# Kernel tuning notes

Hardware: AMD Instinct MI355X
Metric: run time of the kernel (lower is better)

The kernel has to match this reference:

```python
import jax, jax.numpy as jnp
import numpy as np

N_NODES = 4096
N_EDGES = 128
D_X = 128
PE_DIM = 64
NUM_WALKS = 10
WALK_LEN = 5
EMBED_ROWS = 10000
EDGE_P = 0.02
NEG_INF = -1e30


def setup_inputs() -> dict:
    key = jax.random.key(0)
    kx, kh, ke = jax.random.split(key, 3)
    x = jax.random.normal(kx, (N_NODES, D_X), dtype=jnp.float32)
    # binary hypergraph incidence matrix (float, as used by torch H @ H.T)
    incidence = (jax.random.uniform(kh, (N_NODES, N_EDGES)) < EDGE_P).astype(jnp.float32)
    embed_weight = jax.random.normal(ke, (EMBED_ROWS, PE_DIM), dtype=jnp.float32) * 0.02
    return {"x": x, "incidence": incidence, "embed_weight": embed_weight}


def _sample_walks(neighbors, num_walks, walk_length, key):
    """Vectorized random walks: [W, L] node ids and [W, L] validity mask.

    Matches the torch loop: uniform multinomial over (H@H.T>0) neighbors with
    the self-loop zeroed, terminating early when a node has no neighbors.
    """
    N = neighbors.shape[0]
    nb = jax.lax.stop_gradient(neighbors) * (1.0 - jnp.eye(N, dtype=neighbors.dtype))
    logits = jnp.where(nb > 0, 0.0, NEG_INF)  # uniform over neighbors
    row_has = nb.sum(axis=1) > 0              # probs.sum() == 0 -> break
    starts = jnp.repeat(jnp.arange(N), num_walks)  # [W]
    W = starts.shape[0]

    def step(carry, k):
        cur, alive = carry
        alive = alive & row_has[cur]
        nxt = jax.random.categorical(k, logits[cur])  # [W]
        nxt = jnp.where(alive, nxt, cur)
        return (nxt, alive), (nxt, alive)

    keys = jax.random.split(key, walk_length - 1)
    _, (steps, valid) = jax.lax.scan(step, (starts, jnp.ones((W,), bool)), keys)
    walk_nodes = jnp.concatenate([starts[None, :], steps], axis=0).T     # [W, L]
    valid = jnp.concatenate([jnp.ones((1, W), bool), valid], axis=0).T   # [W, L]
    return walk_nodes, valid


def reference(x, incidence, embed_weight):
    N = x.shape[0]
    # node_neighbors = (H @ H.T > 0).float()
    neighbors = ((incidence @ incidence.T) > 0).astype(x.dtype)  # [N, N]
    walk_nodes, valid = _sample_walks(neighbors, NUM_WALKS, WALK_LEN, jax.random.key(42))

    # mean embedding of each walk over its valid (actual) length
    lens = valid.sum(axis=1).astype(x.dtype)                 # [W], >= 1
    emb = embed_weight[walk_nodes]                           # [W, L, D]
    m = (emb * valid[..., None]).sum(axis=1) / lens[:, None]  # [W, D]

    # every (walk, position) occurrence contributes m_walk to pe[node]
    idx = jnp.where(valid, walk_nodes, 0).reshape(-1)                      # [W*L]
    contrib = jnp.where(valid[..., None], m[:, None, :], 0.0)
    contrib = contrib.reshape(-1, m.shape[-1])                             # [W*L, D]
    w = valid.astype(x.dtype).reshape(-1)
    pe_sum = jax.ops.segment_sum(contrib, idx, num_segments=N)             # [N, D]
    cnt = jax.ops.segment_sum(w, idx, num_segments=N)                      # [N]
    pe = jnp.where(cnt[:, None] > 0, pe_sum / jnp.maximum(cnt, 1.0)[:, None], 0.0)
    return jnp.concatenate([x, pe], axis=-1)
```

## Files before the change

### kernel.cpp

```cpp
#include <hip/hip_runtime.h>
#include <hip/hip_fp16.h>
#include <stdint.h>

#define N_NODES   4096
#define N_EDGES   128
#define D_X       128
#define PE_DIM    64
#define NUM_WALKS 10
#define WALK_LEN  5
#define N_WALKS_TOT (N_NODES * NUM_WALKS)
#define OUT_COLS  (D_X + PE_DIM)
#define ROW_CAP   512u
#define VCAP      512u

#define OFF_MASKS   0u
#define OFF_DEG     (OFF_MASKS + N_NODES * 16u)
#define OFF_ADJ     (OFF_DEG + N_NODES * 4u)
#define OFF_WM      (OFF_ADJ + N_NODES * ROW_CAP * 2u)
#define OFF_VCNT    (OFF_WM + N_WALKS_TOT * PE_DIM * 2u)
#define OFF_VLIST   (OFF_VCNT + N_NODES * 4u)

__device__ __forceinline__ void tf2x32(uint32_t kk0, uint32_t kk1,
                                       uint32_t x0, uint32_t x1,
                                       uint32_t& o0, uint32_t& o1) {
  const uint32_t kk2 = kk0 ^ kk1 ^ 0x1BD11BDAu;
  x0 += kk0; x1 += kk1;
  auto rnd = [&](int r) {
    x0 += x1;
    x1 = (x1 << r) | (x1 >> (32 - r));
    x1 ^= x0;
  };
  rnd(13); rnd(15); rnd(26); rnd(6);   x0 += kk1; x1 += kk2 + 1u;
  rnd(17); rnd(29); rnd(16); rnd(24);  x0 += kk2; x1 += kk0 + 2u;
  rnd(13); rnd(15); rnd(26); rnd(6);   x0 += kk0; x1 += kk1 + 3u;
  rnd(17); rnd(29); rnd(16); rnd(24);  x0 += kk1; x1 += kk2 + 4u;
  rnd(13); rnd(15); rnd(26); rnd(6);   x0 += kk2; x1 += kk0 + 5u;
  o0 = x0; o1 = x1;
}

__global__ void k_masks(const float* __restrict__ inc,
                        ulonglong2* __restrict__ masks,
                        unsigned int* __restrict__ vcnt) {
  const int wid = threadIdx.x >> 6, lane = threadIdx.x & 63;
  const int i = blockIdx.x * 4 + wid;
  const float a = inc[i * N_EDGES + lane];
  const float b = inc[i * N_EDGES + 64 + lane];
  const unsigned long long m0 = __ballot(a != 0.f);
  const unsigned long long m1 = __ballot(b != 0.f);
  if (lane == 0) {
    masks[i] = make_ulonglong2(m0, m1);
    vcnt[i] = 0u;
  }
}

__global__ void __launch_bounds__(512)
k_adj(const ulonglong2* __restrict__ masks,
      unsigned short* __restrict__ adj, unsigned int* __restrict__ deg) {
  __shared__ ulonglong2 sm[N_NODES];
  for (int k = threadIdx.x; k < N_NODES; k += 512) sm[k] = masks[k];
  __syncthreads();
  const int wid = threadIdx.x >> 6, lane = threadIdx.x & 63;
  const int i = blockIdx.x * 8 + wid;
  const ulonglong2 mi = sm[i];
  unsigned short* row = adj + (unsigned int)i * ROW_CAP;
  unsigned int base = 0;
  for (int g = 0; g < N_NODES / 64; ++g) {
    const int j = g * 64 + lane;
    const ulonglong2 mj = sm[j];
    const bool pred = (((mi.x & mj.x) | (mi.y & mj.y)) != 0ull) && (j != i);
    const unsigned long long bal = __ballot(pred);
    if (pred) {
      const unsigned int off =
          (unsigned int)__popcll(bal & ((1ull << lane) - 1ull));
      const unsigned int pos = base + off;
      if (pos < ROW_CAP) row[pos] = (unsigned short)j;
    }
    base += (unsigned int)__popcll(bal);
  }
  if (lane == 0) deg[i] = (base < ROW_CAP) ? base : ROW_CAP;
}

__global__ void __launch_bounds__(256)
k_walk(const unsigned int* __restrict__ deg,
       const unsigned short* __restrict__ adj,
       const float* __restrict__ embed,
       __half* __restrict__ walk_m,
       unsigned int* __restrict__ vcnt, unsigned short* __restrict__ vlist) {
  const int wid = threadIdx.x >> 6, lane = threadIdx.x & 63;
  const int w = blockIdx.x * 4 + wid;

  uint32_t a0, a1;
  tf2x32(0u, 42u, (uint32_t)w, (uint32_t)(lane & 1), a0, a1);
  const uint32_t rnd0 = __shfl(a0, 0);
  const uint32_t rnd1 = __shfl(a1, 0);
  const uint32_t rnd2 = __shfl(a0, 1);
  const uint32_t rnd3 = __shfl(a1, 1);

  const uint32_t n0 = (uint32_t)w / NUM_WALKS;
  uint32_t n1, n2, n3, n4, nvalid;
  const unsigned int d0 = deg[n0];
  if (d0 == 0) {
    n1 = n2 = n3 = n4 = n0;
    nvalid = 1u;
  } else {
    uint32_t cur = n0;
    unsigned int d;
    cur = adj[(cur << 9) + (uint32_t)(((uint64_t)rnd0 * d0) >> 32)]; n1 = cur;
    d = deg[cur];
    cur = adj[(cur << 9) + (uint32_t)(((uint64_t)rnd1 * d) >> 32)]; n2 = cur;
    d = deg[cur];
    cur = adj[(cur << 9) + (uint32_t)(((uint64_t)rnd2 * d) >> 32)]; n3 = cur;
    d = deg[cur];
    cur = adj[(cur << 9) + (uint32_t)(((uint64_t)rnd3 * d) >> 32)]; n4 = cur;
    nvalid = 5u;
  }

  float s = embed[n0 * PE_DIM + lane];
  if (nvalid == 5u) {
    s += embed[n1 * PE_DIM + lane];
    s += embed[n2 * PE_DIM + lane];
    s += embed[n3 * PE_DIM + lane];
    s += embed[n4 * PE_DIM + lane];
  }
  const float m = s / (float)nvalid;

  walk_m[(unsigned int)w * PE_DIM + lane] = __float2half(m);

  if ((unsigned int)lane < nvalid) {
    uint32_t node = n0;
    if (lane == 1) node = n1;
    if (lane == 2) node = n2;
    if (lane == 3) node = n3;
    if (lane == 4) node = n4;
    const unsigned int slot = atomicAdd(&vcnt[node], 1u);
    if (slot < VCAP) vlist[node * VCAP + slot] = (unsigned short)w;
  }
}

__global__ void __launch_bounds__(256)
k_gather(const __half* __restrict__ walk_m,
         const unsigned int* __restrict__ vcnt,
         const unsigned short* __restrict__ vlist,
         const float* __restrict__ x,
         float* __restrict__ out) {
  __shared__ float red[4][PE_DIM];
  const int wid = threadIdx.x >> 6, lane = threadIdx.x & 63;
  const int v = blockIdx.x;

  if (wid == 1) {
    const float2 xv = ((const float2*)(x + (unsigned int)v * D_X))[lane];
    ((float2*)(out + (unsigned int)v * OUT_COLS))[lane] = xv;
  }

  unsigned int c = vcnt[v];
  if (c > VCAP) c = VCAP;
  const unsigned short* vl = vlist + (unsigned int)v * VCAP;

  float s = 0.f;
  for (unsigned int base = (unsigned int)wid * 8u; base < c; base += 32u) {
#pragma unroll
    for (int q = 0; q < 8; ++q) {
      const unsigned int idx = base + (unsigned int)q;
      const bool ok = idx < c;
      const unsigned int ww = ok ? (unsigned int)vl[idx] : (unsigned int)vl[0];
      const float val = __half2float(walk_m[ww * PE_DIM + lane]);
      s += ok ? val : 0.f;
    }
  }
  red[wid][lane] = s;
  __syncthreads();
  if (wid == 0) {
    const float t = red[0][lane] + red[1][lane] + red[2][lane] + red[3][lane];
    out[(unsigned int)v * OUT_COLS + D_X + lane] = c ? t / (float)c : 0.f;
  }
}

extern "C" void kernel_launch(void* const* d_in, const int* in_sizes, int n_in,
                              void* d_out, int out_size, void* d_ws, size_t ws_size,
                              hipStream_t stream) {
  const float* x   = (const float*)d_in[0];
  const float* inc = (const float*)d_in[1];
  const float* emb = (const float*)d_in[2];
  float* out = (float*)d_out;

  char* ws = (char*)d_ws;
  ulonglong2*     masks = (ulonglong2*)(ws + OFF_MASKS);
  unsigned int*   deg   = (unsigned int*)(ws + OFF_DEG);
  unsigned short* adj   = (unsigned short*)(ws + OFF_ADJ);
  __half*         wm    = (__half*)(ws + OFF_WM);
  unsigned int*   vcnt  = (unsigned int*)(ws + OFF_VCNT);
  unsigned short* vlist = (unsigned short*)(ws + OFF_VLIST);

  k_masks <<<N_NODES / 4, 256, 0, stream>>>(inc, masks, vcnt);
  k_adj   <<<N_NODES / 8, 512, 0, stream>>>(masks, adj, deg);
  k_walk  <<<N_WALKS_TOT / 4, 256, 0, stream>>>(deg, adj, emb, wm, vcnt, vlist);
  k_gather<<<N_NODES, 256, 0, stream>>>(wm, vcnt, vlist, x, out);
}
```

Measured before the change: 62.29 us.

## Run one walk per thread and recompute walk means in gather from node records

The walk kernel now maps one walk to a thread instead of one walk to a 64-lane wavefront. It stores a compact 16-byte record of the walk's node ids and valid length, no longer computing and writing a half-precision 64-dim mean per walk. The gather kernel reads these records and re-sums the embedding rows for every walk that visits the node, so the per-walk mean is recomputed up to five times. This removes the fp16 rounding and the large intermediate buffer, but gather now makes about five times as many embedding loads per visit, and the walk kernel's lanes diverge on dependent adjacency lookups.

```diff
diff --git a/kernel.cpp b/kernel.cpp
--- a/kernel.cpp
+++ b/kernel.cpp
@@ -1,5 +1,4 @@
 #include <hip/hip_runtime.h>
-#include <hip/hip_fp16.h>
 #include <stdint.h>
 
 #define N_NODES   4096
@@ -16,9 +15,9 @@
 #define OFF_MASKS   0u
 #define OFF_DEG     (OFF_MASKS + N_NODES * 16u)
 #define OFF_ADJ     (OFF_DEG + N_NODES * 4u)
-#define OFF_WM      (OFF_ADJ + N_NODES * ROW_CAP * 2u)
-#define OFF_VCNT    (OFF_WM + N_WALKS_TOT * PE_DIM * 2u)
+#define OFF_VCNT    (OFF_ADJ + N_NODES * ROW_CAP * 2u)
 #define OFF_VLIST   (OFF_VCNT + N_NODES * 4u)
+#define OFF_WNODES  (OFF_VLIST + N_NODES * VCAP * 2u)
 
 __device__ __forceinline__ void tf2x32(uint32_t kk0, uint32_t kk1,
                                        uint32_t x0, uint32_t x1,
@@ -80,23 +79,18 @@
   if (lane == 0) deg[i] = (base < ROW_CAP) ? base : ROW_CAP;
 }
 
-__global__ void __launch_bounds__(256)
+__global__ void __launch_bounds__(64)
 k_walk(const unsigned int* __restrict__ deg,
        const unsigned short* __restrict__ adj,
-       const float* __restrict__ embed,
-       __half* __restrict__ walk_m,
+       uint4* __restrict__ wnodes,
        unsigned int* __restrict__ vcnt, unsigned short* __restrict__ vlist) {
-  const int wid = threadIdx.x >> 6, lane = threadIdx.x & 63;
-  const int w = blockIdx.x * 4 + wid;
-
-  uint32_t a0, a1;
-  tf2x32(0u, 42u, (uint32_t)w, (uint32_t)(lane & 1), a0, a1);
-  const uint32_t rnd0 = __shfl(a0, 0);
-  const uint32_t rnd1 = __shfl(a1, 0);
-  const uint32_t rnd2 = __shfl(a0, 1);
-  const uint32_t rnd3 = __shfl(a1, 1);
-
-  const uint32_t n0 = (uint32_t)w / NUM_WALKS;
+  const uint32_t w = blockIdx.x * 64u + threadIdx.x;
+
+  uint32_t r0, r1, r2, r3;
+  tf2x32(0u, 42u, w, 0u, r0, r1);
+  tf2x32(0u, 42u, w, 1u, r2, r3);
+
+  const uint32_t n0 = w / NUM_WALKS;
   uint32_t n1, n2, n3, n4, nvalid;
   const unsigned int d0 = deg[n0];
   if (d0 == 0) {
@@ -105,51 +99,51 @@
   } else {
     uint32_t cur = n0;
     unsigned int d;
-    cur = adj[(cur << 9) + (uint32_t)(((uint64_t)rnd0 * d0) >> 32)]; n1 = cur;
+    cur = adj[(cur << 9) + (uint32_t)(((uint64_t)r0 * d0) >> 32)]; n1 = cur;
     d = deg[cur];
-    cur = adj[(cur << 9) + (uint32_t)(((uint64_t)rnd1 * d) >> 32)]; n2 = cur;
+    cur = adj[(cur << 9) + (uint32_t)(((uint64_t)r1 * d) >> 32)]; n2 = cur;
     d = deg[cur];
-    cur = adj[(cur << 9) + (uint32_t)(((uint64_t)rnd2 * d) >> 32)]; n3 = cur;
+    cur = adj[(cur << 9) + (uint32_t)(((uint64_t)r2 * d) >> 32)]; n3 = cur;
     d = deg[cur];
-    cur = adj[(cur << 9) + (uint32_t)(((uint64_t)rnd3 * d) >> 32)]; n4 = cur;
+    cur = adj[(cur << 9) + (uint32_t)(((uint64_t)r3 * d) >> 32)]; n4 = cur;
     nvalid = 5u;
   }
 
-  float s = embed[n0 * PE_DIM + lane];
+  uint4 rec;
+  rec.x = n0 | (n1 << 16);
+  rec.y = n2 | (n3 << 16);
+  rec.z = n4 | (nvalid << 16);
+  rec.w = 0u;
+  wnodes[w] = rec;
+
+  unsigned int s0 = atomicAdd(&vcnt[n0], 1u);
+  if (s0 < VCAP) vlist[n0 * VCAP + s0] = (unsigned short)w;
   if (nvalid == 5u) {
-    s += embed[n1 * PE_DIM + lane];
-    s += embed[n2 * PE_DIM + lane];
-    s += embed[n3 * PE_DIM + lane];
-    s += embed[n4 * PE_DIM + lane];
-  }
-  const float m = s / (float)nvalid;
-
-  walk_m[(unsigned int)w * PE_DIM + lane] = __float2half(m);
-
-  if ((unsigned int)lane < nvalid) {
-    uint32_t node = n0;
-    if (lane == 1) node = n1;
-    if (lane == 2) node = n2;
-    if (lane == 3) node = n3;
-    if (lane == 4) node = n4;
-    const unsigned int slot = atomicAdd(&vcnt[node], 1u);
-    if (slot < VCAP) vlist[node * VCAP + slot] = (unsigned short)w;
+    unsigned int s1 = atomicAdd(&vcnt[n1], 1u);
+    if (s1 < VCAP) vlist[n1 * VCAP + s1] = (unsigned short)w;
+    unsigned int s2 = atomicAdd(&vcnt[n2], 1u);
+    if (s2 < VCAP) vlist[n2 * VCAP + s2] = (unsigned short)w;
+    unsigned int s3 = atomicAdd(&vcnt[n3], 1u);
+    if (s3 < VCAP) vlist[n3 * VCAP + s3] = (unsigned short)w;
+    unsigned int s4 = atomicAdd(&vcnt[n4], 1u);
+    if (s4 < VCAP) vlist[n4 * VCAP + s4] = (unsigned short)w;
   }
 }
 
 __global__ void __launch_bounds__(256)
-k_gather(const __half* __restrict__ walk_m,
+k_gather(const uint4* __restrict__ wnodes,
          const unsigned int* __restrict__ vcnt,
          const unsigned short* __restrict__ vlist,
+         const float* __restrict__ embed,
          const float* __restrict__ x,
          float* __restrict__ out) {
   __shared__ float red[4][PE_DIM];
   const int wid = threadIdx.x >> 6, lane = threadIdx.x & 63;
   const int v = blockIdx.x;
 
-  if (wid == 1) {
-    const float2 xv = ((const float2*)(x + (unsigned int)v * D_X))[lane];
-    ((float2*)(out + (unsigned int)v * OUT_COLS))[lane] = xv;
+  if (wid == 3) {
+    const float2 xv = ((const float2*)(x + (size_t)v * D_X))[lane];
+    ((float2*)(out + (size_t)v * OUT_COLS))[lane] = xv;
   }
 
   unsigned int c = vcnt[v];
@@ -157,21 +151,32 @@
   const unsigned short* vl = vlist + (unsigned int)v * VCAP;
 
   float s = 0.f;
-  for (unsigned int base = (unsigned int)wid * 8u; base < c; base += 32u) {
+  for (unsigned int b = (unsigned int)wid * 4u; b < c; b += 16u) {
 #pragma unroll
-    for (int q = 0; q < 8; ++q) {
-      const unsigned int idx = base + (unsigned int)q;
+    for (int q = 0; q < 4; ++q) {
+      const unsigned int idx = b + (unsigned int)q;
       const bool ok = idx < c;
       const unsigned int ww = ok ? (unsigned int)vl[idx] : (unsigned int)vl[0];
-      const float val = __half2float(walk_m[ww * PE_DIM + lane]);
-      s += ok ? val : 0.f;
+      const uint4 rec = wnodes[ww];
+      const uint32_t n0 = rec.x & 0xFFFFu, n1 = rec.x >> 16;
+      const uint32_t n2 = rec.y & 0xFFFFu, n3 = rec.y >> 16;
+      const uint32_t n4 = rec.z & 0xFFFFu, nv = rec.z >> 16;
+      float t = embed[n0 * PE_DIM + lane];
+      if (nv == 5u) {
+        t += embed[n1 * PE_DIM + lane];
+        t += embed[n2 * PE_DIM + lane];
+        t += embed[n3 * PE_DIM + lane];
+        t += embed[n4 * PE_DIM + lane];
+        t *= 0.2f;
+      }
+      s += ok ? t : 0.f;
     }
   }
   red[wid][lane] = s;
   __syncthreads();
   if (wid == 0) {
     const float t = red[0][lane] + red[1][lane] + red[2][lane] + red[3][lane];
-    out[(unsigned int)v * OUT_COLS + D_X + lane] = c ? t / (float)c : 0.f;
+    out[(size_t)v * OUT_COLS + D_X + lane] = c ? t / (float)c : 0.f;
   }
 }
 
@@ -184,15 +189,15 @@
   float* out = (float*)d_out;
 
   char* ws = (char*)d_ws;
-  ulonglong2*     masks = (ulonglong2*)(ws + OFF_MASKS);
-  unsigned int*   deg   = (unsigned int*)(ws + OFF_DEG);
-  unsigned short* adj   = (unsigned short*)(ws + OFF_ADJ);
-  __half*         wm    = (__half*)(ws + OFF_WM);
-  unsigned int*   vcnt  = (unsigned int*)(ws + OFF_VCNT);
-  unsigned short* vlist = (unsigned short*)(ws + OFF_VLIST);
+  ulonglong2*     masks  = (ulonglong2*)(ws + OFF_MASKS);
+  unsigned int*   deg    = (unsigned int*)(ws + OFF_DEG);
+  unsigned short* adj    = (unsigned short*)(ws + OFF_ADJ);
+  unsigned int*   vcnt   = (unsigned int*)(ws + OFF_VCNT);
+  unsigned short* vlist  = (unsigned short*)(ws + OFF_VLIST);
+  uint4*          wnodes = (uint4*)(ws + OFF_WNODES);
 
   k_masks <<<N_NODES / 4, 256, 0, stream>>>(inc, masks, vcnt);
   k_adj   <<<N_NODES / 8, 512, 0, stream>>>(masks, adj, deg);
-  k_walk  <<<N_WALKS_TOT / 4, 256, 0, stream>>>(deg, adj, emb, wm, vcnt, vlist);
-  k_gather<<<N_NODES, 256, 0, stream>>>(wm, vcnt, vlist, x, out);
-}
+  k_walk  <<<N_WALKS_TOT / 64, 64, 0, stream>>>(deg, adj, wnodes, vcnt, vlist);
+  k_gather<<<N_NODES, 256, 0, stream>>>(wnodes, vcnt, vlist, emb, x, out);
+}
```

Result: slower. 80.74 us (+29.6%).

## Build adjacency via per-hyperedge member lists and LDS bitmaps

Applied to the files above, without the earlier changes.

Replaces the all-pairs mask intersection scan, where each node checks all 4096 nodes, with a sparse build. The first kernel appends each node to global per-edge member lists. The adjacency kernel then ORs the members of each incident edge into a shared-memory bitmap and compacts it with a wave prefix scan. This removes the O(N^2) pair check and the 64KB shared-memory mask load per block, at the cost of global atomics and a per-edge capacity cap. The edge counters are reset inside the gather kernel for the next call, so correctness relies on the zero-initialised device globals on the first run.

```diff
diff --git a/kernel.cpp b/kernel.cpp
--- a/kernel.cpp
+++ b/kernel.cpp
@@ -7,18 +7,21 @@
 #define D_X       128
 #define PE_DIM    64
 #define NUM_WALKS 10
-#define WALK_LEN  5
 #define N_WALKS_TOT (N_NODES * NUM_WALKS)
 #define OUT_COLS  (D_X + PE_DIM)
 #define ROW_CAP   512u
 #define VCAP      512u
+#define EMCAP     256
 
 #define OFF_MASKS   0u
 #define OFF_DEG     (OFF_MASKS + N_NODES * 16u)
 #define OFF_ADJ     (OFF_DEG + N_NODES * 4u)
 #define OFF_WM      (OFF_ADJ + N_NODES * ROW_CAP * 2u)
-#define OFF_VCNT    (OFF_WM + N_WALKS_TOT * PE_DIM * 2u)
+#define OFF_VCNT    (OFF_WM + (size_t)N_WALKS_TOT * PE_DIM * 2u)
 #define OFF_VLIST   (OFF_VCNT + N_NODES * 4u)
+
+__device__ unsigned int   g_ecnt[N_EDGES];
+__device__ unsigned short g_emem[N_EDGES * EMCAP];
 
 __device__ __forceinline__ void tf2x32(uint32_t kk0, uint32_t kk1,
                                        uint32_t x0, uint32_t x1,
@@ -38,7 +41,7 @@
   o0 = x0; o1 = x1;
 }
 
-__global__ void k_masks(const float* __restrict__ inc,
+__global__ void k_build(const float* __restrict__ inc,
                         ulonglong2* __restrict__ masks,
                         unsigned int* __restrict__ vcnt) {
   const int wid = threadIdx.x >> 6, lane = threadIdx.x & 63;
@@ -51,33 +54,72 @@
     masks[i] = make_ulonglong2(m0, m1);
     vcnt[i] = 0u;
   }
-}
-
-__global__ void __launch_bounds__(512)
-k_adj(const ulonglong2* __restrict__ masks,
-      unsigned short* __restrict__ adj, unsigned int* __restrict__ deg) {
-  __shared__ ulonglong2 sm[N_NODES];
-  for (int k = threadIdx.x; k < N_NODES; k += 512) sm[k] = masks[k];
+  if (a != 0.f) {
+    const unsigned int s = atomicAdd(&g_ecnt[lane], 1u);
+    if (s < EMCAP) g_emem[(lane << 8) + s] = (unsigned short)i;
+  }
+  if (b != 0.f) {
+    const unsigned int s = atomicAdd(&g_ecnt[64 + lane], 1u);
+    if (s < EMCAP) g_emem[((64 + lane) << 8) + s] = (unsigned short)i;
+  }
+}
+
+__global__ void __launch_bounds__(256)
+k_adjb(const ulonglong2* __restrict__ masks,
+       unsigned short* __restrict__ adj, unsigned int* __restrict__ deg) {
+  __shared__ unsigned int bm[4][N_NODES / 32];
+  const int wid = threadIdx.x >> 6, lane = threadIdx.x & 63;
+  const int i = blockIdx.x * 4 + wid;
+  unsigned int* b = bm[wid];
+  b[lane] = 0u;
+  b[64 + lane] = 0u;
   __syncthreads();
-  const int wid = threadIdx.x >> 6, lane = threadIdx.x & 63;
-  const int i = blockIdx.x * 8 + wid;
-  const ulonglong2 mi = sm[i];
-  unsigned short* row = adj + (unsigned int)i * ROW_CAP;
-  unsigned int base = 0;
-  for (int g = 0; g < N_NODES / 64; ++g) {
-    const int j = g * 64 + lane;
-    const ulonglong2 mj = sm[j];
-    const bool pred = (((mi.x & mj.x) | (mi.y & mj.y)) != 0ull) && (j != i);
-    const unsigned long long bal = __ballot(pred);
-    if (pred) {
-      const unsigned int off =
-          (unsigned int)__popcll(bal & ((1ull << lane) - 1ull));
-      const unsigned int pos = base + off;
-      if (pos < ROW_CAP) row[pos] = (unsigned short)j;
+
+  const ulonglong2 mi = masks[i];
+  unsigned long long mm0 = mi.x, mm1 = mi.y;
+  while (mm0) {
+    const int e = __ffsll(mm0) - 1; mm0 &= mm0 - 1;
+    unsigned int cnt = g_ecnt[e]; if (cnt > EMCAP) cnt = EMCAP;
+    for (unsigned int s = lane; s < cnt; s += 64) {
+      const unsigned int nb = g_emem[(e << 8) + s];
+      if (nb != (unsigned int)i) atomicOr(&b[nb >> 5], 1u << (nb & 31));
     }
-    base += (unsigned int)__popcll(bal);
-  }
-  if (lane == 0) deg[i] = (base < ROW_CAP) ? base : ROW_CAP;
+  }
+  while (mm1) {
+    const int e = 64 + __ffsll(mm1) - 1; mm1 &= mm1 - 1;
+    unsigned int cnt = g_ecnt[e]; if (cnt > EMCAP) cnt = EMCAP;
+    for (unsigned int s = lane; s < cnt; s += 64) {
+      const unsigned int nb = g_emem[(e << 8) + s];
+      if (nb != (unsigned int)i) atomicOr(&b[nb >> 5], 1u << (nb & 31));
+    }
+  }
+  __syncthreads();
+
+  const unsigned int w0 = b[2 * lane], w1 = b[2 * lane + 1];
+  const unsigned int pc = __popc(w0) + __popc(w1);
+  unsigned int pre = pc;
+#pragma unroll
+  for (int d = 1; d < 64; d <<= 1) {
+    const unsigned int t = __shfl_up(pre, d);
+    if (lane >= d) pre += t;
+  }
+  const unsigned int total = __shfl(pre, 63);
+  pre -= pc;
+  unsigned short* row = adj + ((unsigned int)i << 9);
+  unsigned int pos = pre;
+  unsigned int t0 = w0;
+  while (t0) {
+    const int bit = __ffs(t0) - 1; t0 &= t0 - 1;
+    if (pos < ROW_CAP) row[pos] = (unsigned short)(lane * 64 + bit);
+    ++pos;
+  }
+  unsigned int t1 = w1;
+  while (t1) {
+    const int bit = __ffs(t1) - 1; t1 &= t1 - 1;
+    if (pos < ROW_CAP) row[pos] = (unsigned short)(lane * 64 + 32 + bit);
+    ++pos;
+  }
+  if (lane == 63) deg[i] = (total < ROW_CAP) ? total : ROW_CAP;
 }
 
 __global__ void __launch_bounds__(256)
@@ -124,7 +166,7 @@
   }
   const float m = s / (float)nvalid;
 
-  walk_m[(unsigned int)w * PE_DIM + lane] = __float2half(m);
+  walk_m[(size_t)w * PE_DIM + lane] = __float2half(m);
 
   if ((unsigned int)lane < nvalid) {
     uint32_t node = n0;
@@ -147,9 +189,11 @@
   const int wid = threadIdx.x >> 6, lane = threadIdx.x & 63;
   const int v = blockIdx.x;
 
-  if (wid == 1) {
-    const float2 xv = ((const float2*)(x + (unsigned int)v * D_X))[lane];
-    ((float2*)(out + (unsigned int)v * OUT_COLS))[lane] = xv;
+  if (v == 0 && threadIdx.x < N_EDGES) g_ecnt[threadIdx.x] = 0u;
+
+  if (wid == 3) {
+    const float2 xv = ((const float2*)(x + (size_t)v * D_X))[lane];
+    ((float2*)(out + (size_t)v * OUT_COLS))[lane] = xv;
   }
 
   unsigned int c = vcnt[v];
@@ -163,7 +207,7 @@
       const unsigned int idx = base + (unsigned int)q;
       const bool ok = idx < c;
       const unsigned int ww = ok ? (unsigned int)vl[idx] : (unsigned int)vl[0];
-      const float val = __half2float(walk_m[ww * PE_DIM + lane]);
+      const float val = __half2float(walk_m[(size_t)ww * PE_DIM + lane]);
       s += ok ? val : 0.f;
     }
   }
@@ -171,7 +215,7 @@
   __syncthreads();
   if (wid == 0) {
     const float t = red[0][lane] + red[1][lane] + red[2][lane] + red[3][lane];
-    out[(unsigned int)v * OUT_COLS + D_X + lane] = c ? t / (float)c : 0.f;
+    out[(size_t)v * OUT_COLS + D_X + lane] = c ? t / (float)c : 0.f;
   }
 }
 
@@ -191,8 +235,8 @@
   unsigned int*   vcnt  = (unsigned int*)(ws + OFF_VCNT);
   unsigned short* vlist = (unsigned short*)(ws + OFF_VLIST);
 
-  k_masks <<<N_NODES / 4, 256, 0, stream>>>(inc, masks, vcnt);
-  k_adj   <<<N_NODES / 8, 512, 0, stream>>>(masks, adj, deg);
+  k_build <<<N_NODES / 4, 256, 0, stream>>>(inc, masks, vcnt);
+  k_adjb  <<<N_NODES / 4, 256, 0, stream>>>(masks, adj, deg);
   k_walk  <<<N_WALKS_TOT / 4, 256, 0, stream>>>(deg, adj, emb, wm, vcnt, vlist);
   k_gather<<<N_NODES, 256, 0, stream>>>(wm, vcnt, vlist, x, out);
 }
```

After: 86.82 us. 39.4% more time.
